# Performance work log

Hardware: AMD Instinct MI355X
Metric: run time of the kernel (lower is better)

The kernel has to match this reference:

```python
import jax, jax.numpy as jnp
import numpy as np

# Hyperparameters matching init_kwargs
IN_CH = 64
OUT_CH = 128
KERNEL = (3, 3)
STRIDE = (1, 1)
PADDING = 'SAME'
K_ORDER = 3          # spline order
G_INTERVALS = 3      # grid intervals
GRID_MIN, GRID_MAX = -1.0, 1.0
N_BASIS = G_INTERVALS + K_ORDER  # basis functions per input = 6
PATCH_DIM = IN_CH * KERNEL[0] * KERNEL[1]  # 576


def _grid():
    # Extended uniform knot vector: G + 2k + 1 knots
    h = (GRID_MAX - GRID_MIN) / G_INTERVALS
    return jnp.arange(-K_ORDER, G_INTERVALS + K_ORDER + 1, dtype=jnp.float32) * h + GRID_MIN


def _b_splines(x):
    # x: [N, n_in] -> bases: [N, n_in, G + k]
    grid = _grid()  # [G + 2k + 1]
    xe = x[..., None]  # [N, n_in, 1]
    bases = ((xe >= grid[:-1]) & (xe < grid[1:])).astype(x.dtype)  # order-0, [N, n_in, G+2k]
    for p in range(1, K_ORDER + 1):
        left = (xe - grid[: -(p + 1)]) / (grid[p:-1] - grid[: -(p + 1)]) * bases[..., :-1]
        right = (grid[p + 1:] - xe) / (grid[p + 1:] - grid[1:-p]) * bases[..., 1:]
        bases = left + right
    return bases  # [N, n_in, G + k]


def setup_inputs() -> dict:
    key = jax.random.key(0)
    k0, k1, k2, k3 = jax.random.split(key, 4)
    x = jax.random.normal(k0, (8, 64, 64, IN_CH), dtype=jnp.float32)
    base_w = jax.random.normal(k1, (OUT_CH, PATCH_DIM), dtype=jnp.float32) * 0.05
    spline_w = jax.random.normal(k2, (OUT_CH, PATCH_DIM, N_BASIS), dtype=jnp.float32) * 0.05
    bias = jax.random.normal(k3, (OUT_CH,), dtype=jnp.float32) * 0.05
    return {'x': x, 'base_w': base_w, 'spline_w': spline_w, 'bias': bias}


def reference(x, base_w, spline_w, bias):
    batch = x.shape[0]
    dn = ('NHWC', 'HWIO', 'NHWC')
    patches = jax.lax.conv_general_dilated_patches(
        lhs=x, filter_shape=KERNEL, window_strides=STRIDE, padding=PADDING,
        dimension_numbers=dn)  # [B, H, W, patch_dim]
    out_spatial = patches.shape[1:-1]
    p = patches.reshape(-1, PATCH_DIM)  # [N, patch_dim]
    # EfficientKAN: residual (silu) branch + spline branch + bias
    base_out = jax.nn.silu(p) @ base_w.T                      # [N, out]
    bases = _b_splines(p)                                      # [N, patch_dim, G+k]
    spline_out = jnp.einsum('nig,oig->no', bases, spline_w)    # [N, out]
    y = base_out + spline_out + bias
    return y.reshape(batch, *out_spatial, OUT_CH)
```

## Files before the change

### kernel.cpp

```cpp
#include <hip/hip_runtime.h>

typedef __attribute__((ext_vector_type(8))) short short8;
typedef __attribute__((ext_vector_type(16))) float f32x16;

#define FT2_SHORTS (512u * 4356u * 8u)
#define PLANE16    4356

typedef __attribute__((address_space(3))) unsigned int lds_u32_t;
typedef __attribute__((address_space(1))) const unsigned int g_u32_t;

__device__ __forceinline__ unsigned short f2bf(float x) {
    union { float f; unsigned u; } v; v.f = x;
    unsigned r = v.u + 0x7FFFu + ((v.u >> 16) & 1u);
    return (unsigned short)(r >> 16);
}

__device__ __forceinline__ void feat8(float p, unsigned short* uf) {
    float e   = __expf(-p);
    float sig = 1.f / (1.f + e);
    uf[0] = f2bf(p * sig);
    float u  = p * 1.5f + 4.5f;
    float fj = floorf(u);
    int   j0 = (int)fj;
    float t  = u - fj;
    bool  inr = (u >= 0.f) && (u < 9.f);
    float t2 = t * t, t3 = t2 * t;
    const float c16 = 1.f / 6.f;
    float r0 = t3 * c16;
    float r1 = (-3.f * t3 + 3.f * t2 + 3.f * t + 1.f) * c16;
    float r2 = (3.f * t3 - 6.f * t2 + 4.f) * c16;
    float s1 = 1.f - t;
    float r3 = s1 * s1 * s1 * c16;
#pragma unroll
    for (int g = 0; g < 6; ++g) {
        int r = j0 - g;
        float v = (r == 0) ? r0 : ((r == 1) ? r1 : ((r == 2) ? r2 : ((r == 3) ? r3 : 0.f)));
        uf[1 + g] = f2bf(inr ? v : 0.f);
    }
    uf[7] = 0;
}

__global__ __launch_bounds__(256)
void prep_all(const float* __restrict__ x,
              const float* __restrict__ bw, const float* __restrict__ sw,
              unsigned short* __restrict__ ft, unsigned short* __restrict__ wt) {
    const int blk = blockIdx.x;
    const int tid = threadIdx.x;

    if (tid < 144) {
        int idx = blk * 144 + tid;
        int o = idx / 576;
        int i = idx - o * 576;
        int slab = i >> 3, e = i & 7;
        union { unsigned short u[8]; uint4 v; } pk;
        pk.u[0] = f2bf(bw[o * 576 + i]);
        const float* s = sw + (size_t)(o * 576 + i) * 6;
#pragma unroll
        for (int f = 0; f < 6; ++f) pk.u[1 + f] = f2bf(s[f]);
        pk.u[7] = 0;
        *(uint4*)(wt + ((size_t)slab * 8192 + e * 1024 + o * 8)) = pk.v;
    }

    {
        short8 pad = { 0, 0, (short)0x3CAB, (short)0x3EF5,
                       (short)0x3EF5, (short)0x3CAB, 0, 0 };
        for (int t = tid; t < 260; t += 256) {
            int yy, xx;
            if (t < 66)       { yy = 0;       xx = t; }
            else if (t < 132) { yy = 65;      xx = t - 66; }
            else if (t < 196) { yy = t - 131; xx = 0; }
            else              { yy = t - 195; xx = 65; }
            ((short8*)ft)[blk * PLANE16 + yy * 66 + xx] = pad;
        }
    }

    __shared__ float Xl[64 * 65];
    const int b = blk >> 6, y = blk & 63;
    const float* xl = x + (size_t)blk * 4096;
    for (int f4 = tid; f4 < 1024; f4 += 256) {
        float4 v = ((const float4*)xl)[f4];
        int xx = f4 >> 4, c4 = (f4 & 15) << 2;
        float* d = &Xl[xx * 65 + c4];
        d[0] = v.x; d[1] = v.y; d[2] = v.z; d[3] = v.w;
    }
    __syncthreads();
    const int xx = tid & 63;
    const int cw = tid >> 6;
#pragma unroll 4
    for (int p = 0; p < 16; ++p) {
        int c = cw + (p << 2);
        float pv = Xl[xx * 65 + c];
        union { unsigned short u[8]; uint4 v; } pk;
        feat8(pv, pk.u);
        size_t o16 = (size_t)(c * 8 + b) * PLANE16 + (y + 1) * 66 + (xx + 1);
        *(uint4*)(ft + (o16 << 3)) = pk.v;
    }
}

#define STAGE_AB(sl)                                                                  \
    {                                                                                 \
        unsigned short* bufb = Bufs + (((sl) & 1) << 14);                             \
        const unsigned short* bsrc = wt + (size_t)(slab0 + (sl)) * 8192 + bsoff;      \
        unsigned short* bdst = bufb + bsoff;                                          \
        _Pragma("unroll")                                                             \
        for (int t = 0; t < 4; ++t)                                                   \
            __builtin_amdgcn_global_load_lds((g_u32_t*)(bsrc + t * 512),              \
                                             (lds_u32_t*)(bdst + t * 512), 16, 0, 0); \
        _Pragma("unroll")                                                             \
        for (int t = 0; t < 4; ++t) {                                                 \
            int idx = wave * 4 + t;                                                   \
            int ia  = (slab0 + (sl)) * 8 + (idx >> 1);                                \
            int g2  = idx & 1;                                                        \
            int c_  = (ia * 7282) >> 16;                                              \
            int i9_ = ia - c_ * 9;                                                    \
            int kh_ = (i9_ * 11) >> 5;                                                \
            int kw_ = i9_ - kh_ * 3;                                                  \
            const unsigned short* asrc = ft +                                         \
                (((size_t)(c_ * 8 + b) * PLANE16 + (y0 + g2 + kh_) * 66 + kw_) << 3)  \
                + lane * 8;                                                           \
            unsigned short* adst = bufb + 8192 + idx * 512 + lane * 8;                \
            __builtin_amdgcn_global_load_lds((g_u32_t*)asrc, (lds_u32_t*)adst,        \
                                             16, 0, 0);                               \
        }                                                                             \
    }

#define KSTEP(s_)                                                                     \
    {                                                                                 \
        int iloc = 2 * (s_) + h;                                                      \
        const unsigned short* Ab = bufr + 8192 + (iloc * 2 + g) * 512;                \
        const unsigned short* Bb = bufr + iloc * 1024;                                \
        short8 a0 = *(const short8*)(Ab + l32 * 8);                                   \
        short8 a1 = *(const short8*)(Ab + (32 + l32) * 8);                            \
        short8 b0 = *(const short8*)(Bb + (nh * 64 + l32) * 8);                       \
        short8 b1 = *(const short8*)(Bb + (nh * 64 + 32 + l32) * 8);                  \
        acc00 = __builtin_amdgcn_mfma_f32_32x32x16_bf16(a0, b0, acc00, 0, 0, 0);      \
        acc01 = __builtin_amdgcn_mfma_f32_32x32x16_bf16(a0, b1, acc01, 0, 0, 0);      \
        acc10 = __builtin_amdgcn_mfma_f32_32x32x16_bf16(a1, b0, acc10, 0, 0, 0);      \
        acc11 = __builtin_amdgcn_mfma_f32_32x32x16_bf16(a1, b1, acc11, 0, 0, 0);      \
    }

__global__ __launch_bounds__(256, 2)
void convkan_gemm(const unsigned short* __restrict__ ft,
                  const unsigned short* __restrict__ wt,
                  const float* __restrict__ bias,
                  float* __restrict__ out) {
    extern __shared__ unsigned short Bufs[];

    const int tid  = threadIdx.x;
    const int blk  = blockIdx.x;
    const int kk   = blk & 1;
    const int mb   = blk >> 1;
    const int lane = tid & 63;
    const int wave = tid >> 6;
    const int g    = wave >> 1;
    const int nh   = wave & 1;
    const int l32  = lane & 31;
    const int h    = lane >> 5;

    const int b  = mb >> 5;
    const int y0 = (mb & 31) << 1;
    const int slab0 = kk * 36;

    const int bsoff = wave * 2048 + lane * 8;

    f32x16 acc00, acc01, acc10, acc11;
#pragma unroll
    for (int e = 0; e < 16; ++e) { acc00[e] = 0.f; acc01[e] = 0.f; acc10[e] = 0.f; acc11[e] = 0.f; }

    STAGE_AB(0);
    __syncthreads();

    for (int it = 0; it < 36; ++it) {
        if (it + 1 < 36) STAGE_AB(it + 1);
        const unsigned short* bufr = Bufs + ((it & 1) << 14);
        KSTEP(0) KSTEP(1) KSTEP(2) KSTEP(3)
        __syncthreads();
    }

    const float bv0 = kk ? 0.f : bias[nh * 64 + l32];
    const float bv1 = kk ? 0.f : bias[nh * 64 + 32 + l32];
    const int prow = (mb * 2 + g) * 64;
    const int ncol = nh * 64 + l32;
#pragma unroll
    for (int r = 0; r < 16; ++r) {
        int mrow = (r & 3) + ((r >> 2) << 3) + 4 * h;
        float* p0 = out + (size_t)(prow + mrow) * 128 + ncol;
        float* p1 = out + (size_t)(prow + 32 + mrow) * 128 + ncol;
        atomicAdd(p0,      acc00[r] + bv0);
        atomicAdd(p0 + 32, acc01[r] + bv1);
        atomicAdd(p1,      acc10[r] + bv0);
        atomicAdd(p1 + 32, acc11[r] + bv1);
    }
}

extern "C" void kernel_launch(void* const* d_in, const int* in_sizes, int n_in,
                              void* d_out, int out_size, void* d_ws, size_t ws_size,
                              hipStream_t stream) {
    (void)in_sizes; (void)n_in; (void)ws_size;
    const float* x        = (const float*)d_in[0];
    const float* base_w   = (const float*)d_in[1];
    const float* spline_w = (const float*)d_in[2];
    const float* bias     = (const float*)d_in[3];
    float* out = (float*)d_out;

    unsigned short* ft = (unsigned short*)d_ws;
    unsigned short* wt = ft + FT2_SHORTS;

    hipMemsetAsync(out, 0, (size_t)out_size * sizeof(float), stream);
    hipLaunchKernelGGL(prep_all, dim3(512), dim3(256), 0, stream,
                       x, base_w, spline_w, ft, wt);

    const int shmem = 2 * 16384 * 2;
    (void)hipFuncSetAttribute((const void*)convkan_gemm,
                              hipFuncAttributeMaxDynamicSharedMemorySize, shmem);
    hipLaunchKernelGGL(convkan_gemm, dim3(512), dim3(256), shmem, stream,
                       ft, wt, bias, out);
}
```

Measured before the change: 148.9 us.

## Load A operands directly to registers and fold output zeroing into prep kernel

The GEMM kernel now loads the activation (A) fragments straight from global memory into registers, double-buffered across two register arrays. Only the weights are staged through LDS, in larger 16-slab chunks, so the loop runs 18 iterations instead of 36 and needs fewer barriers. The weight layout becomes a simple [i][o] order, and zeroing the output moves from a separate hipMemsetAsync into the prep kernel, which removes one launch. The cost is much higher register pressure from 32 short8 A fragments per thread, which risks spills or lower occupancy, and the A reads lose the LDS-based sharing between waves.

New measurement: 152.9 us. +2.7%, slower.

```diff
diff --git a/kernel.cpp b/kernel.cpp
--- a/kernel.cpp
+++ b/kernel.cpp
@@ -43,22 +43,28 @@
 __global__ __launch_bounds__(256)
 void prep_all(const float* __restrict__ x,
               const float* __restrict__ bw, const float* __restrict__ sw,
-              unsigned short* __restrict__ ft, unsigned short* __restrict__ wt) {
+              unsigned short* __restrict__ ft, unsigned short* __restrict__ wt,
+              float* __restrict__ out) {
     const int blk = blockIdx.x;
     const int tid = threadIdx.x;
+
+    {
+        float4 z4 = make_float4(0.f, 0.f, 0.f, 0.f);
+        float4* ob = (float4*)(out + (size_t)blk * 64 * 128);
+        for (int t = tid; t < 2048; t += 256) ob[t] = z4;
+    }
 
     if (tid < 144) {
         int idx = blk * 144 + tid;
         int o = idx / 576;
         int i = idx - o * 576;
-        int slab = i >> 3, e = i & 7;
         union { unsigned short u[8]; uint4 v; } pk;
         pk.u[0] = f2bf(bw[o * 576 + i]);
         const float* s = sw + (size_t)(o * 576 + i) * 6;
 #pragma unroll
         for (int f = 0; f < 6; ++f) pk.u[1 + f] = f2bf(s[f]);
         pk.u[7] = 0;
-        *(uint4*)(wt + ((size_t)slab * 8192 + e * 1024 + o * 8)) = pk.v;
+        *(uint4*)(wt + ((size_t)(i * 128 + o) * 8)) = pk.v;
     }
 
     {
@@ -97,54 +103,54 @@
     }
 }
 
-#define STAGE_AB(sl)                                                                  \
-    {                                                                                 \
-        unsigned short* bufb = Bufs + (((sl) & 1) << 14);                             \
-        const unsigned short* bsrc = wt + (size_t)(slab0 + (sl)) * 8192 + bsoff;      \
-        unsigned short* bdst = bufb + bsoff;                                          \
-        _Pragma("unroll")                                                             \
-        for (int t = 0; t < 4; ++t)                                                   \
-            __builtin_amdgcn_global_load_lds((g_u32_t*)(bsrc + t * 512),              \
-                                             (lds_u32_t*)(bdst + t * 512), 16, 0, 0); \
-        _Pragma("unroll")                                                             \
-        for (int t = 0; t < 4; ++t) {                                                 \
-            int idx = wave * 4 + t;                                                   \
-            int ia  = (slab0 + (sl)) * 8 + (idx >> 1);                                \
-            int g2  = idx & 1;                                                        \
-            int c_  = (ia * 7282) >> 16;                                              \
-            int i9_ = ia - c_ * 9;                                                    \
-            int kh_ = (i9_ * 11) >> 5;                                                \
-            int kw_ = i9_ - kh_ * 3;                                                  \
-            const unsigned short* asrc = ft +                                         \
-                (((size_t)(c_ * 8 + b) * PLANE16 + (y0 + g2 + kh_) * 66 + kw_) << 3)  \
-                + lane * 8;                                                           \
-            unsigned short* adst = bufb + 8192 + idx * 512 + lane * 8;                \
-            __builtin_amdgcn_global_load_lds((g_u32_t*)asrc, (lds_u32_t*)adst,        \
-                                             16, 0, 0);                               \
-        }                                                                             \
-    }
-
-#define KSTEP(s_)                                                                     \
-    {                                                                                 \
-        int iloc = 2 * (s_) + h;                                                      \
-        const unsigned short* Ab = bufr + 8192 + (iloc * 2 + g) * 512;                \
-        const unsigned short* Bb = bufr + iloc * 1024;                                \
-        short8 a0 = *(const short8*)(Ab + l32 * 8);                                   \
-        short8 a1 = *(const short8*)(Ab + (32 + l32) * 8);                            \
-        short8 b0 = *(const short8*)(Bb + (nh * 64 + l32) * 8);                       \
-        short8 b1 = *(const short8*)(Bb + (nh * 64 + 32 + l32) * 8);                  \
-        acc00 = __builtin_amdgcn_mfma_f32_32x32x16_bf16(a0, b0, acc00, 0, 0, 0);      \
-        acc01 = __builtin_amdgcn_mfma_f32_32x32x16_bf16(a0, b1, acc01, 0, 0, 0);      \
-        acc10 = __builtin_amdgcn_mfma_f32_32x32x16_bf16(a1, b0, acc10, 0, 0, 0);      \
-        acc11 = __builtin_amdgcn_mfma_f32_32x32x16_bf16(a1, b1, acc11, 0, 0, 0);      \
-    }
+#define STAGE(sl)                                                                     \
+  {                                                                                   \
+    char* dst = (char*)Bs + (((sl) & 1) << 15) + epair * 16384 + bn * 16;             \
+    const char* src = (const char*)wt + ((size_t)(ebase + (sl) * 16 + epair * 8)      \
+                                         << 11) + bn * 16;                            \
+    _Pragma("unroll")                                                                 \
+    for (int j = 0; j < 8; ++j)                                                       \
+        __builtin_amdgcn_global_load_lds((g_u32_t*)(src + j * 2048),                  \
+                                         (lds_u32_t*)(dst + j * 2048), 16, 0, 0);     \
+  }
+
+#define ALOAD(sl, ARR)                                                                \
+  {                                                                                   \
+    _Pragma("unroll")                                                                 \
+    for (int s_ = 0; s_ < 8; ++s_) {                                                  \
+        int i_  = ebase + (sl) * 16 + 2 * s_ + h;                                     \
+        int c_  = (i_ * 7282) >> 16;                                                  \
+        int i9_ = i_ - c_ * 9;                                                        \
+        int kh_ = (i9_ * 11) >> 5;                                                    \
+        int kw_ = i9_ - kh_ * 3;                                                      \
+        int t16 = c_ * (8 * PLANE16) + kh_ * 66 + kw_ + abase;                        \
+        ARR[2 * s_]     = fptr[t16];                                                  \
+        ARR[2 * s_ + 1] = fptr[t16 + 32];                                             \
+    }                                                                                 \
+  }
+
+#define KSTEP(s_, ARR, bufp)                                                          \
+  {                                                                                   \
+    const char* Bb = (const char*)Bs + ((bufp) << 15) + (2 * (s_) + h) * 2048         \
+                     + (nh * 64 + l32) * 16;                                          \
+    short8 b0 = *(const short8*)(Bb);                                                 \
+    short8 b1 = *(const short8*)(Bb + 512);                                           \
+    acc00 = __builtin_amdgcn_mfma_f32_32x32x16_bf16(ARR[2*(s_)],   b0, acc00, 0,0,0); \
+    acc01 = __builtin_amdgcn_mfma_f32_32x32x16_bf16(ARR[2*(s_)],   b1, acc01, 0,0,0); \
+    acc10 = __builtin_amdgcn_mfma_f32_32x32x16_bf16(ARR[2*(s_)+1], b0, acc10, 0,0,0); \
+    acc11 = __builtin_amdgcn_mfma_f32_32x32x16_bf16(ARR[2*(s_)+1], b1, acc11, 0,0,0); \
+  }
+
+#define KSTEPS(ARR, bufp) \
+    KSTEP(0, ARR, bufp) KSTEP(1, ARR, bufp) KSTEP(2, ARR, bufp) KSTEP(3, ARR, bufp) \
+    KSTEP(4, ARR, bufp) KSTEP(5, ARR, bufp) KSTEP(6, ARR, bufp) KSTEP(7, ARR, bufp)
 
 __global__ __launch_bounds__(256, 2)
 void convkan_gemm(const unsigned short* __restrict__ ft,
                   const unsigned short* __restrict__ wt,
                   const float* __restrict__ bias,
                   float* __restrict__ out) {
-    extern __shared__ unsigned short Bufs[];
+    __shared__ unsigned short Bs[2 * 16 * 128 * 8];
 
     const int tid  = threadIdx.x;
     const int blk  = blockIdx.x;
@@ -159,22 +165,33 @@
 
     const int b  = mb >> 5;
     const int y0 = (mb & 31) << 1;
-    const int slab0 = kk * 36;
-
-    const int bsoff = wave * 2048 + lane * 8;
+    const int ebase = kk * 288;
+
+    const int abase = b * PLANE16 + (y0 + g) * 66 + l32;
+    const short8* fptr = (const short8*)ft;
+
+    const int bn    = tid & 127;
+    const int epair = tid >> 7;
 
     f32x16 acc00, acc01, acc10, acc11;
 #pragma unroll
     for (int e = 0; e < 16; ++e) { acc00[e] = 0.f; acc01[e] = 0.f; acc10[e] = 0.f; acc11[e] = 0.f; }
 
-    STAGE_AB(0);
-    __syncthreads();
-
-    for (int it = 0; it < 36; ++it) {
-        if (it + 1 < 36) STAGE_AB(it + 1);
-        const unsigned short* bufr = Bufs + ((it & 1) << 14);
-        KSTEP(0) KSTEP(1) KSTEP(2) KSTEP(3)
+    short8 aA[16], aB[16];
+    STAGE(0);
+    ALOAD(0, aA);
+
+    for (int it = 0; it < 18; it += 2) {
         __syncthreads();
+        STAGE(it + 1);
+        ALOAD(it + 1, aB);
+        KSTEPS(aA, 0)
+        __syncthreads();
+        if (it + 2 < 18) {
+            STAGE(it + 2);
+            ALOAD(it + 2, aA);
+        }
+        KSTEPS(aB, 1)
     }
 
     const float bv0 = kk ? 0.f : bias[nh * 64 + l32];
@@ -196,7 +213,7 @@
 extern "C" void kernel_launch(void* const* d_in, const int* in_sizes, int n_in,
                               void* d_out, int out_size, void* d_ws, size_t ws_size,
                               hipStream_t stream) {
-    (void)in_sizes; (void)n_in; (void)ws_size;
+    (void)in_sizes; (void)n_in; (void)out_size; (void)ws_size;
     const float* x        = (const float*)d_in[0];
     const float* base_w   = (const float*)d_in[1];
     const float* spline_w = (const float*)d_in[2];
@@ -206,13 +223,8 @@
     unsigned short* ft = (unsigned short*)d_ws;
     unsigned short* wt = ft + FT2_SHORTS;
 
-    hipMemsetAsync(out, 0, (size_t)out_size * sizeof(float), stream);
     hipLaunchKernelGGL(prep_all, dim3(512), dim3(256), 0, stream,
-                       x, base_w, spline_w, ft, wt);
-
-    const int shmem = 2 * 16384 * 2;
-    (void)hipFuncSetAttribute((const void*)convkan_gemm,
-                              hipFuncAttributeMaxDynamicSharedMemorySize, shmem);
-    hipLaunchKernelGGL(convkan_gemm, dim3(512), dim3(256), shmem, stream,
+                       x, base_w, spline_w, ft, wt, out);
+    hipLaunchKernelGGL(convkan_gemm, dim3(512), dim3(256), 0, stream,
                        ft, wt, bias, out);
 }
```
